# Performance work log

Measured on AMD Instinct MI355X. Metric: run time of the kernel, lower is better.

The kernel has to match this reference:

```python
import jax, jax.numpy as jnp
import numpy as np

# Haar (db1) decomposition filters, pywt convention
_S = 1.0 / np.sqrt(2.0)
# dec_lo = [s, s], dec_hi = [-s, s]. Each scalar input v becomes signal [v, 0]
# (zero-pad to 2**dwt_level = 2). The single valid DWT coeff (mode='zero') is
#   cA = v * dec_lo[1] = v * s ;  cD = v * dec_hi[1] = v * s
CA_COEF = np.float32(_S)   # dec_lo[1]
CD_COEF = np.float32(_S)   # dec_hi[1]

B, N, F, OUT = 8, 20000, 256, 256
WAVELET_FULL_LEN = 2  # len(cA) + len(cD) for level-1 db1 on length-2 signal


def setup_inputs() -> dict:
    key = jax.random.key(0)
    kx, kw, kb, kwo, kbo = jax.random.split(key, 5)
    x = jax.random.normal(kx, (B, N, F), dtype=jnp.float32)
    # per-feature nn.Linear(wavelet_full_len, 1) stacked: weight [F, 2], bias [F]
    lim_nl = 1.0 / np.sqrt(WAVELET_FULL_LEN)
    W_nl = jax.random.uniform(kw, (F, WAVELET_FULL_LEN), jnp.float32, -lim_nl, lim_nl)
    b_nl = jax.random.uniform(kb, (F,), jnp.float32, -lim_nl, lim_nl)
    # linear_out: [out_dim, feat_dim] torch layout, bias [out_dim]
    lim_o = 1.0 / np.sqrt(F)
    W_out = jax.random.uniform(kwo, (OUT, F), jnp.float32, -lim_o, lim_o)
    b_out = jax.random.uniform(kbo, (OUT,), jnp.float32, -lim_o, lim_o)
    return {"x": x, "W_nl": W_nl, "b_nl": b_nl, "W_out": W_out, "b_out": b_out}


def reference(x, W_nl, b_nl, W_out, b_out):
    # Batched wavelet features: for each scalar, coeffs are [cA, cD] = [s*v, s*v]
    # feat_wave: [B, N, F, 2]
    feat_wave = jnp.stack([x * CA_COEF, x * CD_COEF], axis=-1)
    # Per-feature Linear(2, 1), batched over the feature dim
    agg_nl = jnp.einsum("bnfk,fk->bnf", feat_wave, W_nl) + b_nl  # [B, N, F]
    # Output linear (dropout is identity in eval)
    out = jnp.einsum("bnf,of->bno", agg_nl, W_out) + b_out  # [B, N, OUT]
    return out
```

## Files before the change

### kernel.cpp

```cpp
#include <hip/hip_runtime.h>

typedef __bf16 bf16x8 __attribute__((ext_vector_type(8)));
typedef float f32x4 __attribute__((ext_vector_type(4)));
typedef unsigned short ushort8 __attribute__((ext_vector_type(8)));

__device__ __forceinline__ unsigned short f2b(float f) {
    unsigned int u = __float_as_uint(f);
    return (unsigned short)((u + 0x7fffu + ((u >> 16) & 1u)) >> 16);
}

__device__ __forceinline__ void gl_lds16(const void* g, void* l) {
    __builtin_amdgcn_global_load_lds(
        (const __attribute__((address_space(1))) unsigned int*)g,
        (__attribute__((address_space(3))) unsigned int*)l, 16, 0, 0);
}

__global__ __launch_bounds__(256) void wk_prep(
    const float* __restrict__ Wnl, const float* __restrict__ bnl,
    const float* __restrict__ Wout, const float* __restrict__ bout,
    unsigned short* __restrict__ wfrag, float* __restrict__ wbias) {
    int b = blockIdx.x, tid = threadIdx.x;
    if (b < 256) {
        int t = b * 256 + tid;
        int j = t & 7;
        int lane = (t >> 3) & 63;
        int ks = (t >> 9) & 7;
        int ct = t >> 12;
        int f = ks * 32 + ((lane >> 4) << 3) + j;
        int o = ct * 16 + (lane & 15);
        float c = 0.70710678f * (Wnl[2 * f] + Wnl[2 * f + 1]);
        wfrag[t] = f2b(c * Wout[o * 256 + f]);
    } else {
        int o = tid;
        const float4* wr = (const float4*)(Wout + o * 256);
        const float4* bn = (const float4*)bnl;
        float s = 0.f;
        #pragma unroll 4
        for (int i = 0; i < 64; ++i) {
            float4 a = bn[i], b4 = wr[i];
            s += a.x * b4.x + a.y * b4.y + a.z * b4.z + a.w * b4.w;
        }
        wbias[o] = bout[o] + s;
    }
}

__global__ __launch_bounds__(512, 2) void wk_main(
    const float* __restrict__ x, const unsigned short* __restrict__ wfrag,
    const float* __restrict__ wbias, float* __restrict__ out) {
    const int tid  = threadIdx.x;
    const int lane = tid & 63;
    const int w    = tid >> 6;
    const int m    = lane & 15;
    const int quad = lane >> 4;
    const int swz  = m & 7;

    __shared__ float4 Xlds[2][4096];

    const int b  = blockIdx.x;
    const int t0 = (b * 2500) >> 8;
    const int t1 = ((b + 1) * 2500) >> 8;

    int4  Wf[2][8];
    f32x4 bias[2];
    {
        const int4* ws = (const int4*)wfrag;
        #pragma unroll
        for (int c2 = 0; c2 < 2; ++c2) {
            #pragma unroll
            for (int ks = 0; ks < 8; ++ks)
                Wf[c2][ks] = ws[(((2 * w + c2) * 8 + ks) << 6) + lane];
            bias[c2] = *(const f32x4*)(wbias + (2 * w + c2) * 16 + quad * 4);
        }
    }

    const char* xc = (const char*)x;
    #define STAGE(T, P)                                                        \
        {                                                                      \
            _Pragma("unroll")                                                  \
            for (int s = 0; s < 8; ++s) {                                      \
                int r = s * 8 + w;                                             \
                gl_lds16(xc + (size_t)((T) * 64 + r) * 1024 + ((lane ^ w) << 4),\
                         (void*)&Xlds[P][s * 512 + w * 64]);                   \
            }                                                                  \
        }

    STAGE(t0, 0);
    STAGE(t0 + 1, 1);
    asm volatile("s_waitcnt vmcnt(8)" ::: "memory");
    __builtin_amdgcn_s_barrier();
    __builtin_amdgcn_sched_barrier(0);

    int t = t0, p = 0;
    while (true) {
        const float4* buf = (const float4*)Xlds[p];
        #pragma unroll
        for (int mt = 0; mt < 4; ++mt) {
            f32x4 a0 = bias[0], a1 = bias[1];
            const int rb = (mt * 16 + m) * 64;
            #pragma unroll
            for (int ks = 0; ks < 8; ++ks) {
                float4 u = buf[rb + ((ks * 8 + quad * 2)     ^ swz)];
                float4 v = buf[rb + ((ks * 8 + quad * 2 + 1) ^ swz)];
                ushort8 sh;
                sh[0] = f2b(u.x); sh[1] = f2b(u.y); sh[2] = f2b(u.z); sh[3] = f2b(u.w);
                sh[4] = f2b(v.x); sh[5] = f2b(v.y); sh[6] = f2b(v.z); sh[7] = f2b(v.w);
                bf16x8 afr = __builtin_bit_cast(bf16x8, sh);
                a0 = __builtin_amdgcn_mfma_f32_16x16x32_bf16(
                    __builtin_bit_cast(bf16x8, Wf[0][ks]), afr, a0, 0, 0, 0);
                a1 = __builtin_amdgcn_mfma_f32_16x16x32_bf16(
                    __builtin_bit_cast(bf16x8, Wf[1][ks]), afr, a1, 0, 0, 0);
            }
            float* op = out + (size_t)(t * 64 + mt * 16 + m) * 256 + w * 32 + quad * 4;
            *(f32x4*)op        = a0;
            *(f32x4*)(op + 16) = a1;
        }

        if (++t == t1) break;
        __builtin_amdgcn_s_barrier();
        __builtin_amdgcn_sched_barrier(0);
        if (t + 1 < t1) {
            STAGE(t + 1, p);
            asm volatile("s_waitcnt vmcnt(16)" ::: "memory");
        } else {
            asm volatile("s_waitcnt vmcnt(8)" ::: "memory");
        }
        __builtin_amdgcn_s_barrier();
        __builtin_amdgcn_sched_barrier(0);
        p ^= 1;
    }
    #undef STAGE
}

extern "C" void kernel_launch(void* const* d_in, const int* in_sizes, int n_in,
                              void* d_out, int out_size, void* d_ws, size_t ws_size,
                              hipStream_t stream) {
    const float* x    = (const float*)d_in[0];
    const float* Wnl  = (const float*)d_in[1];
    const float* bnl  = (const float*)d_in[2];
    const float* Wout = (const float*)d_in[3];
    const float* bout = (const float*)d_in[4];

    unsigned short* wfrag = (unsigned short*)d_ws;
    float* wbias = (float*)((char*)d_ws + 131072);

    wk_prep<<<257, 256, 0, stream>>>(Wnl, bnl, Wout, bout, wfrag, wbias);
    wk_main<<<256, 512, 0, stream>>>(x, wfrag, wbias, (float*)d_out);
}
```

Before: 309.5 us.

## Stage x through registers, convert to bf16 once into padded LDS

Replaces the direct global-to-LDS fp32 staging with register-prefetched loads that are converted to bf16 once and written into a padded LDS layout. MFMA operands are then read directly as bf16x8 with no per-use conversion. Tile height drops to 32 rows and the grid doubles to 512 blocks with higher occupancy bounds. The intent is to cut LDS traffic and redundant conversion work and to improve latency hiding. In exchange it relies on register prefetch rather than async copies and adds a per-tile barrier.

```diff
diff --git a/kernel.cpp b/kernel.cpp
--- a/kernel.cpp
+++ b/kernel.cpp
@@ -1,18 +1,12 @@
 #include <hip/hip_runtime.h>
 
 typedef __bf16 bf16x8 __attribute__((ext_vector_type(8)));
+typedef __bf16 bf16x4 __attribute__((ext_vector_type(4)));
 typedef float f32x4 __attribute__((ext_vector_type(4)));
-typedef unsigned short ushort8 __attribute__((ext_vector_type(8)));
 
 __device__ __forceinline__ unsigned short f2b(float f) {
     unsigned int u = __float_as_uint(f);
     return (unsigned short)((u + 0x7fffu + ((u >> 16) & 1u)) >> 16);
-}
-
-__device__ __forceinline__ void gl_lds16(const void* g, void* l) {
-    __builtin_amdgcn_global_load_lds(
-        (const __attribute__((address_space(1))) unsigned int*)g,
-        (__attribute__((address_space(3))) unsigned int*)l, 16, 0, 0);
 }
 
 __global__ __launch_bounds__(256) void wk_prep(
@@ -44,7 +38,7 @@
     }
 }
 
-__global__ __launch_bounds__(512, 2) void wk_main(
+__global__ __launch_bounds__(512, 4) void wk_main(
     const float* __restrict__ x, const unsigned short* __restrict__ wfrag,
     const float* __restrict__ wbias, float* __restrict__ out) {
     const int tid  = threadIdx.x;
@@ -52,13 +46,12 @@
     const int w    = tid >> 6;
     const int m    = lane & 15;
     const int quad = lane >> 4;
-    const int swz  = m & 7;
 
-    __shared__ float4 Xlds[2][4096];
+    __shared__ char Xlds[2][18432];
 
     const int b  = blockIdx.x;
-    const int t0 = (b * 2500) >> 8;
-    const int t1 = ((b + 1) * 2500) >> 8;
+    const int t0 = (b * 5000) >> 9;
+    const int t1 = ((b + 1) * 5000) >> 9;
 
     int4  Wf[2][8];
     f32x4 bias[2];
@@ -73,62 +66,53 @@
         }
     }
 
-    const char* xc = (const char*)x;
-    #define STAGE(T, P)                                                        \
-        {                                                                      \
-            _Pragma("unroll")                                                  \
-            for (int s = 0; s < 8; ++s) {                                      \
-                int r = s * 8 + w;                                             \
-                gl_lds16(xc + (size_t)((T) * 64 + r) * 1024 + ((lane ^ w) << 4),\
-                         (void*)&Xlds[P][s * 512 + w * 64]);                   \
-            }                                                                  \
+    f32x4 sbuf[4];
+    #define LOADT(T)                                                          \
+        {                                                                     \
+            const f32x4* xt = (const f32x4*)x + (size_t)(T) * 2048;           \
+            _Pragma("unroll")                                                 \
+            for (int s = 0; s < 4; ++s)                                       \
+                sbuf[s] = xt[s * 512 + w * 64 + lane];                        \
         }
 
-    STAGE(t0, 0);
-    STAGE(t0 + 1, 1);
-    asm volatile("s_waitcnt vmcnt(8)" ::: "memory");
-    __builtin_amdgcn_s_barrier();
-    __builtin_amdgcn_sched_barrier(0);
+    LOADT(t0);
+    int p = 0;
+    for (int t = t0; t < t1; ++t) {
+        {
+            char* dst = Xlds[p] + w * 576 + lane * 8;
+            #pragma unroll
+            for (int s = 0; s < 4; ++s) {
+                f32x4 u = sbuf[s];
+                bf16x4 h;
+                h[0] = (__bf16)u[0]; h[1] = (__bf16)u[1];
+                h[2] = (__bf16)u[2]; h[3] = (__bf16)u[3];
+                *(bf16x4*)(dst + s * 4608) = h;
+            }
+        }
+        if (t + 1 < t1) LOADT(t + 1);
+        asm volatile("s_waitcnt lgkmcnt(0)" ::: "memory");
+        __builtin_amdgcn_s_barrier();
+        __builtin_amdgcn_sched_barrier(0);
 
-    int t = t0, p = 0;
-    while (true) {
-        const float4* buf = (const float4*)Xlds[p];
+        const char* src = Xlds[p] + m * 576 + quad * 16;
         #pragma unroll
-        for (int mt = 0; mt < 4; ++mt) {
+        for (int mt = 0; mt < 2; ++mt) {
             f32x4 a0 = bias[0], a1 = bias[1];
-            const int rb = (mt * 16 + m) * 64;
             #pragma unroll
             for (int ks = 0; ks < 8; ++ks) {
-                float4 u = buf[rb + ((ks * 8 + quad * 2)     ^ swz)];
-                float4 v = buf[rb + ((ks * 8 + quad * 2 + 1) ^ swz)];
-                ushort8 sh;
-                sh[0] = f2b(u.x); sh[1] = f2b(u.y); sh[2] = f2b(u.z); sh[3] = f2b(u.w);
-                sh[4] = f2b(v.x); sh[5] = f2b(v.y); sh[6] = f2b(v.z); sh[7] = f2b(v.w);
-                bf16x8 afr = __builtin_bit_cast(bf16x8, sh);
+                bf16x8 afr = *(const bf16x8*)(src + mt * 9216 + ks * 64);
                 a0 = __builtin_amdgcn_mfma_f32_16x16x32_bf16(
                     __builtin_bit_cast(bf16x8, Wf[0][ks]), afr, a0, 0, 0, 0);
                 a1 = __builtin_amdgcn_mfma_f32_16x16x32_bf16(
                     __builtin_bit_cast(bf16x8, Wf[1][ks]), afr, a1, 0, 0, 0);
             }
-            float* op = out + (size_t)(t * 64 + mt * 16 + m) * 256 + w * 32 + quad * 4;
+            float* op = out + (size_t)(t * 32 + mt * 16 + m) * 256 + w * 32 + quad * 4;
             *(f32x4*)op        = a0;
             *(f32x4*)(op + 16) = a1;
         }
-
-        if (++t == t1) break;
-        __builtin_amdgcn_s_barrier();
-        __builtin_amdgcn_sched_barrier(0);
-        if (t + 1 < t1) {
-            STAGE(t + 1, p);
-            asm volatile("s_waitcnt vmcnt(16)" ::: "memory");
-        } else {
-            asm volatile("s_waitcnt vmcnt(8)" ::: "memory");
-        }
-        __builtin_amdgcn_s_barrier();
-        __builtin_amdgcn_sched_barrier(0);
         p ^= 1;
     }
-    #undef STAGE
+    #undef LOADT
 }
 
 extern "C" void kernel_launch(void* const* d_in, const int* in_sizes, int n_in,
@@ -144,5 +128,5 @@
     float* wbias = (float*)((char*)d_ws + 131072);
 
     wk_prep<<<257, 256, 0, stream>>>(Wnl, bnl, Wout, bout, wfrag, wbias);
-    wk_main<<<256, 512, 0, stream>>>(x, wfrag, wbias, (float*)d_out);
+    wk_main<<<512, 512, 0, stream>>>(x, wfrag, wbias, (float*)d_out);
 }
```

Measured after the change: 302.4 us. -2.3%, faster.
